# Performance work log

Hardware: AMD Instinct MI355X
Metric: run time of the kernel (lower is better)

The kernel has to match this reference:

```python
import jax, jax.numpy as jnp
import numpy as np

ALG_DIM = 248      # dim of E8 adjoint rep
NNZ_BASE = 300     # base structure-constant triples (antisymmetrized -> 600 nnz)
N_NODES = 20000
N_EDGES = 160000


def _structure_constants():
    """Deterministic sparse antisymmetric structure constants C_ijk.

    Returns index arrays (ci, cj, ck) int32 and values cv float32 such that
    [x, y]_k = sum_t cv[t] * x[ci[t]] * y[cj[t]] with C antisymmetric in (i, j).
    """
    rng = np.random.default_rng(0)
    i = rng.integers(0, ALG_DIM, NNZ_BASE)
    j = rng.integers(0, ALG_DIM, NNZ_BASE)
    j = np.where(j == i, (j + 1) % ALG_DIM, j)  # bracket of equal basis elts is 0
    k = rng.integers(0, ALG_DIM, NNZ_BASE)
    v = rng.normal(size=NNZ_BASE).astype(np.float32)
    ci = np.concatenate([i, j]).astype(np.int32)
    cj = np.concatenate([j, i]).astype(np.int32)
    ck = np.concatenate([k, k]).astype(np.int32)
    cv = np.concatenate([v, -v]).astype(np.float32)
    return jnp.asarray(ci), jnp.asarray(cj), jnp.asarray(ck), jnp.asarray(cv)


def _bracket(x, y, ci, cj, ck, cv):
    """Sparse Lie bracket [x, y]: x, y have shape (..., ALG_DIM)."""
    terms = x[..., ci] * y[..., cj] * cv          # (..., nnz)
    return jnp.zeros(x.shape, x.dtype).at[..., ck].add(terms)


def setup_inputs() -> dict:
    key = jax.random.key(0)
    k1, k2 = jax.random.split(key)
    features = jax.random.normal(k1, (N_NODES, ALG_DIM), dtype=jnp.float32)
    edge_index = jax.random.randint(k2, (2, N_EDGES), 0, N_NODES, dtype=jnp.int32)
    ci, cj, ck, cv = _structure_constants()
    return {
        "features": features,
        "edge_index": edge_index,
        "ci": ci, "cj": cj, "ck": ck, "cv": cv,
        "alpha_msg": jnp.float32(1.0),     # msg_projection.alpha
        "alpha_bil": jnp.float32(1.0),     # msg_bilinear.alpha
        "alpha_w": jnp.float32(1.0),       # update_W.alpha
        "update_scale": jnp.float32(0.1),
    }


def reference(features, edge_index, ci, cj, ck, cv,
              alpha_msg, alpha_bil, alpha_w, update_scale):
    src_idx = edge_index[0]
    tgt_idx = edge_index[1]
    src = features[src_idx]                        # (E, d) gather
    tgt = features[tgt_idx]                        # (E, d) gather
    # message: alpha_bil * [alpha_msg * src, tgt]
    msg = alpha_bil * _bracket(alpha_msg * src, tgt, ci, cj, ck, cv)
    # scatter-add aggregate into per-node accumulator
    agg = jnp.zeros_like(features).at[tgt_idx].add(msg)
    # bracket-based update: x + agg + scale * [agg, alpha_w * agg]
    upd = _bracket(agg, alpha_w * agg, ci, cj, ck, cv)
    return features + agg + update_scale * upd
```

## Files before the change

### kernel.cpp

```cpp
#include <hip/hip_runtime.h>


#define ALG    248
#define ALG4    62
#define PIT2    64
#define SLOTS   32
#define WPB      4
#define NBLK  2048
#define TPL     10
#define NPAD   640

__device__ __forceinline__ unsigned bf16rne(float f) {
    const unsigned u = __float_as_uint(f);
    return (u + 0x7fffu + ((u >> 16) & 1u)) >> 16;
}

__global__ __launch_bounds__(256) void elc_fill(
    const int* __restrict__ ei, int E, int N,
    int* __restrict__ cnt, int* __restrict__ slot,
    const float* __restrict__ feat, uint2* __restrict__ bfeat,
    const int* __restrict__ ci, const int* __restrict__ cj,
    const int* __restrict__ ck, const float* __restrict__ cv,
    int* __restrict__ g_tij, float* __restrict__ g_tv, int nnz)
{
    const int tid = threadIdx.x;

    if (blockIdx.x == 0) {
        __shared__ int   s_cnt[256];
        __shared__ int   s_scan[256];
        __shared__ int   s_cur[256];
        __shared__ int   ls_k[NPAD];
        __shared__ int   ls_ij[NPAD];
        __shared__ float ls_v[NPAD];

        s_cnt[tid] = 0;
        for (int t = tid; t < NPAD; t += 256) { ls_k[t] = 0; ls_ij[t] = 0; ls_v[t] = 0.f; }
        __syncthreads();
        for (int t = tid; t < nnz; t += 256) atomicAdd(&s_cnt[ck[t]], 1);
        __syncthreads();
        int v = s_cnt[tid];
        s_scan[tid] = v;
        __syncthreads();
        for (int off = 1; off < 256; off <<= 1) {
            int u = (tid >= off) ? s_scan[tid - off] : 0;
            __syncthreads();
            s_scan[tid] += u;
            __syncthreads();
        }
        s_cur[tid] = s_scan[tid] - v;
        __syncthreads();
        for (int t = tid; t < nnz; t += 256) {
            const int k = ck[t];
            const int p = atomicAdd(&s_cur[k], 1);
            ls_k[p]  = k;
            ls_ij[p] = ci[t] | (cj[t] << 8);
            ls_v[p]  = cv[t];
        }
        __syncthreads();
        for (int p = tid; p < NPAD; p += 256) {
            const int k  = ls_k[p];
            const int fl = (p + 1 < NPAD && ls_k[p + 1] == k) ? 0 : 1;
            const int w  = ls_ij[p] | (k << 16) | (fl << 24);
            const int phys = (p % TPL) * 64 + (p / TPL);
            g_tij[phys] = w;
            g_tv[phys]  = ls_v[p];
        }
    }

    for (int e = blockIdx.x * 256 + tid; e < E; e += gridDim.x * 256) {
        const int t = ei[E + e];
        const int p = atomicAdd(&cnt[t], 1);
        if (p < SLOTS) slot[t * SLOTS + p] = ei[e];
    }

    const float4* feat4 = (const float4*)feat;
    const int items = N * PIT2;
    for (int it = blockIdx.x * 256 + tid; it < items; it += gridDim.x * 256) {
        const int n = it >> 6;
        const int g = it & 63;
        uint2 o = make_uint2(0u, 0u);
        if (g < ALG4) {
            const float4 f = feat4[(size_t)n * ALG4 + g];
            o.x = bf16rne(f.x) | (bf16rne(f.y) << 16);
            o.y = bf16rne(f.z) | (bf16rne(f.w) << 16);
        }
        bfeat[(size_t)n * PIT2 + g] = o;
    }
}

__global__ __launch_bounds__(256) void elc_node(
    const float* __restrict__ feat,
    const uint2* __restrict__ bfeat,
    const int*   __restrict__ cnt,
    const int*   __restrict__ slot,
    const int*   __restrict__ g_tij,
    const float* __restrict__ g_tv,
    const float* __restrict__ p_am, const float* __restrict__ p_ab,
    const float* __restrict__ p_aw, const float* __restrict__ p_us,
    float* __restrict__ out, int N)
{
    __shared__ __align__(16) float s_tg[WPB][ALG];
    __shared__ __align__(16) float s_S[WPB][ALG];
    __shared__ float s_ag[WPB][ALG];

    const int tid  = threadIdx.x;
    const int lane = tid & 63;
    const int wave = tid >> 6;
    const float4* feat4 = (const float4*)feat;

    int   tw[TPL];
    float tv[TPL];
#pragma unroll
    for (int d = 0; d < TPL; ++d) {
        tw[d] = g_tij[d * 64 + lane];
        tv[d] = g_tv[d * 64 + lane];
    }

    const float cab   = (*p_ab) * (*p_am);
    const float scale = (*p_us) * (*p_aw);

    float* tg = s_tg[wave];
    float* S  = s_S[wave];
    float* ag = s_ag[wave];

    const int stride = NBLK * WPB;
    int n = blockIdx.x * WPB + wave;

    int deg_c = 0, sn_c = 0;
    float4 tgt_c = make_float4(0.f, 0.f, 0.f, 0.f);
    if (n < N) {
        deg_c = min(cnt[n], SLOTS);
        sn_c  = slot[n * SLOTS + (lane & 31)];
        if (lane < ALG4) tgt_c = feat4[(size_t)n * ALG4 + lane];
    }

    int    nP   = -1;
    float4 accP = make_float4(0.f, 0.f, 0.f, 0.f);
    float4 tgtP = make_float4(0.f, 0.f, 0.f, 0.f);

    while (true) {
        const bool have_cur = (n < N);
        const int  n_next   = n + stride;

        uint2 f[8];
        if (have_cur) {
#pragma unroll
            for (int d = 0; d < 8; ++d) {
                f[d] = make_uint2(0u, 0u);
                const int sd = __shfl(sn_c, d);
                if (d < deg_c && lane < ALG4)
                    f[d] = bfeat[(size_t)sd * PIT2 + lane];
            }
        }

        int deg_n = 0, sn_n = 0;
        float4 tgt_n = make_float4(0.f, 0.f, 0.f, 0.f);
        if (have_cur && n_next < N) {
            deg_n = min(cnt[n_next], SLOTS);
            sn_n  = slot[n_next * SLOTS + (lane & 31)];
            if (lane < ALG4) tgt_n = feat4[(size_t)n_next * ALG4 + lane];
        }

        if (nP >= 0) {
            if (lane < ALG4) {
                ((float4*)tg)[lane] = tgtP;
                ((float4*)S)[lane]  = accP;
            }
#pragma unroll
            for (int q = 0; q < 4; ++q) {
                const int k = lane + 64 * q;
                if (k < ALG) ag[k] = 0.f;
            }
            float acc = 0.f;
#pragma unroll
            for (int d = 0; d < TPL; ++d) {
                const int w = tw[d];
                const int i = w & 255;
                const int j = (w >> 8) & 255;
                acc = fmaf(tv[d] * S[i], tg[j], acc);
                if ((w & (1 << 24)) || d == TPL - 1) {
                    atomicAdd(&ag[(w >> 16) & 255], cab * acc);
                    acc = 0.f;
                }
            }
#pragma unroll
            for (int q = 0; q < 4; ++q) {
                const int k = lane + 64 * q;
                if (k < ALG) S[k] = tg[k] + ag[k];
            }
            float acc2 = 0.f;
#pragma unroll
            for (int d = 0; d < TPL; ++d) {
                const int w = tw[d];
                const int i = w & 255;
                const int j = (w >> 8) & 255;
                acc2 = fmaf(tv[d] * ag[i], ag[j], acc2);
                if ((w & (1 << 24)) || d == TPL - 1) {
                    atomicAdd(&S[(w >> 16) & 255], scale * acc2);
                    acc2 = 0.f;
                }
            }
#pragma unroll
            for (int q = 0; q < 4; ++q) {
                const int k = lane + 64 * q;
                if (k < ALG)
                    out[(size_t)nP * ALG + k] = S[k];
            }
        }

        if (!have_cur) break;

        float4 acc = make_float4(0.f, 0.f, 0.f, 0.f);
#pragma unroll
        for (int d = 0; d < 8; ++d) {
            acc.x += __uint_as_float(f[d].x << 16);
            acc.y += __uint_as_float(f[d].x & 0xffff0000u);
            acc.z += __uint_as_float(f[d].y << 16);
            acc.w += __uint_as_float(f[d].y & 0xffff0000u);
        }
        for (int d = 8; d < deg_c; ++d) {
            const int sd = __shfl(sn_c, d);
            if (lane < ALG4) {
                const uint2 fd = bfeat[(size_t)sd * PIT2 + lane];
                acc.x += __uint_as_float(fd.x << 16);
                acc.y += __uint_as_float(fd.x & 0xffff0000u);
                acc.z += __uint_as_float(fd.y << 16);
                acc.w += __uint_as_float(fd.y & 0xffff0000u);
            }
        }

        nP = n; accP = acc; tgtP = tgt_c;
        n = n_next; deg_c = deg_n; sn_c = sn_n; tgt_c = tgt_n;
    }
}

extern "C" void kernel_launch(void* const* d_in, const int* in_sizes, int n_in,
                              void* d_out, int out_size, void* d_ws, size_t ws_size,
                              hipStream_t stream) {
    const float* feat = (const float*)d_in[0];
    const int*   ei   = (const int*)d_in[1];
    const int*   ci   = (const int*)d_in[2];
    const int*   cj   = (const int*)d_in[3];
    const int*   ck   = (const int*)d_in[4];
    const float* cv   = (const float*)d_in[5];
    const float* p_am = (const float*)d_in[6];
    const float* p_ab = (const float*)d_in[7];
    const float* p_aw = (const float*)d_in[8];
    const float* p_us = (const float*)d_in[9];
    float* out = (float*)d_out;

    const int N   = in_sizes[0] / ALG;
    const int E   = in_sizes[1] / 2;
    const int nnz = in_sizes[5];

    char* w = (char*)d_ws;
    int*   g_tij = (int*)w;               w += (size_t)NPAD * sizeof(int);
    float* g_tv  = (float*)w;             w += (size_t)NPAD * sizeof(float);
    int*   cnt   = (int*)w;               w += (size_t)N * sizeof(int);
    int*   slot  = (int*)w;               w += (size_t)N * SLOTS * sizeof(int);
    uint2* bfeat = (uint2*)w;

    hipMemsetAsync(cnt, 0, (size_t)N * sizeof(int), stream);

    elc_fill<<<1024, 256, 0, stream>>>(ei, E, N, cnt, slot, feat, bfeat,
                                       ci, cj, ck, cv, g_tij, g_tv, nnz);
    elc_node<<<NBLK, 256, 0, stream>>>(feat, bfeat, cnt, slot, g_tij, g_tv,
                                       p_am, p_ab, p_aw, p_us, out, N);
}
```

Before: 164.0 us.

## Split fill kernel, read target features as bf16, halve waves per block

Splits the combined setup kernel into separate pack, convert and bucket kernels. The node kernel now reads target-node features from the bf16 copy instead of fp32, halving that traffic, and runs with 2 waves per block over twice as many blocks. This adds kernel launches and loses precision on target features, which may also affect the residual output term.

Result: no change. 166.8 us (+1.7%).

```diff
diff --git a/kernel.cpp b/kernel.cpp
--- a/kernel.cpp
+++ b/kernel.cpp
@@ -5,8 +5,8 @@
 #define ALG4    62
 #define PIT2    64
 #define SLOTS   32
-#define WPB      4
-#define NBLK  2048
+#define WPB      2
+#define NBLK  4096
 #define TPL     10
 #define NPAD   640
 
@@ -15,67 +15,60 @@
     return (u + 0x7fffu + ((u >> 16) & 1u)) >> 16;
 }
 
-__global__ __launch_bounds__(256) void elc_fill(
-    const int* __restrict__ ei, int E, int N,
-    int* __restrict__ cnt, int* __restrict__ slot,
-    const float* __restrict__ feat, uint2* __restrict__ bfeat,
+__global__ __launch_bounds__(256) void elc_pack(
     const int* __restrict__ ci, const int* __restrict__ cj,
     const int* __restrict__ ck, const float* __restrict__ cv,
     int* __restrict__ g_tij, float* __restrict__ g_tv, int nnz)
 {
+    __shared__ int   s_cnt[256];
+    __shared__ int   s_scan[256];
+    __shared__ int   s_cur[256];
+    __shared__ int   ls_k[NPAD];
+    __shared__ int   ls_ij[NPAD];
+    __shared__ float ls_v[NPAD];
     const int tid = threadIdx.x;
 
-    if (blockIdx.x == 0) {
-        __shared__ int   s_cnt[256];
-        __shared__ int   s_scan[256];
-        __shared__ int   s_cur[256];
-        __shared__ int   ls_k[NPAD];
-        __shared__ int   ls_ij[NPAD];
-        __shared__ float ls_v[NPAD];
-
-        s_cnt[tid] = 0;
-        for (int t = tid; t < NPAD; t += 256) { ls_k[t] = 0; ls_ij[t] = 0; ls_v[t] = 0.f; }
+    s_cnt[tid] = 0;
+    for (int t = tid; t < NPAD; t += 256) { ls_k[t] = 0; ls_ij[t] = 0; ls_v[t] = 0.f; }
+    __syncthreads();
+    for (int t = tid; t < nnz; t += 256) atomicAdd(&s_cnt[ck[t]], 1);
+    __syncthreads();
+    int v = s_cnt[tid];
+    s_scan[tid] = v;
+    __syncthreads();
+    for (int off = 1; off < 256; off <<= 1) {
+        int u = (tid >= off) ? s_scan[tid - off] : 0;
         __syncthreads();
-        for (int t = tid; t < nnz; t += 256) atomicAdd(&s_cnt[ck[t]], 1);
+        s_scan[tid] += u;
         __syncthreads();
-        int v = s_cnt[tid];
-        s_scan[tid] = v;
-        __syncthreads();
-        for (int off = 1; off < 256; off <<= 1) {
-            int u = (tid >= off) ? s_scan[tid - off] : 0;
-            __syncthreads();
-            s_scan[tid] += u;
-            __syncthreads();
-        }
-        s_cur[tid] = s_scan[tid] - v;
-        __syncthreads();
-        for (int t = tid; t < nnz; t += 256) {
-            const int k = ck[t];
-            const int p = atomicAdd(&s_cur[k], 1);
-            ls_k[p]  = k;
-            ls_ij[p] = ci[t] | (cj[t] << 8);
-            ls_v[p]  = cv[t];
-        }
-        __syncthreads();
-        for (int p = tid; p < NPAD; p += 256) {
-            const int k  = ls_k[p];
-            const int fl = (p + 1 < NPAD && ls_k[p + 1] == k) ? 0 : 1;
-            const int w  = ls_ij[p] | (k << 16) | (fl << 24);
-            const int phys = (p % TPL) * 64 + (p / TPL);
-            g_tij[phys] = w;
-            g_tv[phys]  = ls_v[p];
-        }
-    }
-
-    for (int e = blockIdx.x * 256 + tid; e < E; e += gridDim.x * 256) {
-        const int t = ei[E + e];
-        const int p = atomicAdd(&cnt[t], 1);
-        if (p < SLOTS) slot[t * SLOTS + p] = ei[e];
-    }
-
+    }
+    s_cur[tid] = s_scan[tid] - v;
+    __syncthreads();
+    for (int t = tid; t < nnz; t += 256) {
+        const int k = ck[t];
+        const int p = atomicAdd(&s_cur[k], 1);
+        ls_k[p]  = k;
+        ls_ij[p] = ci[t] | (cj[t] << 8);
+        ls_v[p]  = cv[t];
+    }
+    __syncthreads();
+    for (int p = tid; p < NPAD; p += 256) {
+        const int k  = ls_k[p];
+        const int fl = (p + 1 < NPAD && ls_k[p + 1] == k) ? 0 : 1;
+        const int w  = ls_ij[p] | (k << 16) | (fl << 24);
+        const int phys = (p % TPL) * 64 + (p / TPL);
+        g_tij[phys] = w;
+        g_tv[phys]  = ls_v[p];
+    }
+}
+
+__global__ __launch_bounds__(256) void elc_convert(
+    const float* __restrict__ feat, uint2* __restrict__ bfeat, int N)
+{
     const float4* feat4 = (const float4*)feat;
     const int items = N * PIT2;
-    for (int it = blockIdx.x * 256 + tid; it < items; it += gridDim.x * 256) {
+    for (int it = blockIdx.x * 256 + threadIdx.x; it < items;
+         it += gridDim.x * 256) {
         const int n = it >> 6;
         const int g = it & 63;
         uint2 o = make_uint2(0u, 0u);
@@ -88,8 +81,18 @@
     }
 }
 
-__global__ __launch_bounds__(256) void elc_node(
-    const float* __restrict__ feat,
+__global__ __launch_bounds__(256) void elc_bucket(
+    const int* __restrict__ ei, int E,
+    int* __restrict__ cnt, int* __restrict__ slot)
+{
+    for (int e = blockIdx.x * 256 + threadIdx.x; e < E; e += gridDim.x * 256) {
+        const int t = ei[E + e];
+        const int p = atomicAdd(&cnt[t], 1);
+        if (p < SLOTS) slot[t * SLOTS + p] = ei[e];
+    }
+}
+
+__global__ __launch_bounds__(128) void elc_node(
     const uint2* __restrict__ bfeat,
     const int*   __restrict__ cnt,
     const int*   __restrict__ slot,
@@ -106,7 +109,6 @@
     const int tid  = threadIdx.x;
     const int lane = tid & 63;
     const int wave = tid >> 6;
-    const float4* feat4 = (const float4*)feat;
 
     int   tw[TPL];
     float tv[TPL];
@@ -127,16 +129,16 @@
     int n = blockIdx.x * WPB + wave;
 
     int deg_c = 0, sn_c = 0;
-    float4 tgt_c = make_float4(0.f, 0.f, 0.f, 0.f);
+    uint2 tgt_c = make_uint2(0u, 0u);
     if (n < N) {
         deg_c = min(cnt[n], SLOTS);
         sn_c  = slot[n * SLOTS + (lane & 31)];
-        if (lane < ALG4) tgt_c = feat4[(size_t)n * ALG4 + lane];
-    }
-
-    int    nP   = -1;
+        if (lane < ALG4) tgt_c = bfeat[(size_t)n * PIT2 + lane];
+    }
+
+    int   nP   = -1;
     float4 accP = make_float4(0.f, 0.f, 0.f, 0.f);
-    float4 tgtP = make_float4(0.f, 0.f, 0.f, 0.f);
+    uint2  tgtP = make_uint2(0u, 0u);
 
     while (true) {
         const bool have_cur = (n < N);
@@ -154,16 +156,21 @@
         }
 
         int deg_n = 0, sn_n = 0;
-        float4 tgt_n = make_float4(0.f, 0.f, 0.f, 0.f);
+        uint2 tgt_n = make_uint2(0u, 0u);
         if (have_cur && n_next < N) {
             deg_n = min(cnt[n_next], SLOTS);
             sn_n  = slot[n_next * SLOTS + (lane & 31)];
-            if (lane < ALG4) tgt_n = feat4[(size_t)n_next * ALG4 + lane];
+            if (lane < ALG4) tgt_n = bfeat[(size_t)n_next * PIT2 + lane];
         }
 
         if (nP >= 0) {
             if (lane < ALG4) {
-                ((float4*)tg)[lane] = tgtP;
+                float4 tf;
+                tf.x = __uint_as_float(tgtP.x << 16);
+                tf.y = __uint_as_float(tgtP.x & 0xffff0000u);
+                tf.z = __uint_as_float(tgtP.y << 16);
+                tf.w = __uint_as_float(tgtP.y & 0xffff0000u);
+                ((float4*)tg)[lane] = tf;
                 ((float4*)S)[lane]  = accP;
             }
 #pragma unroll
@@ -262,8 +269,9 @@
 
     hipMemsetAsync(cnt, 0, (size_t)N * sizeof(int), stream);
 
-    elc_fill<<<1024, 256, 0, stream>>>(ei, E, N, cnt, slot, feat, bfeat,
-                                       ci, cj, ck, cv, g_tij, g_tv, nnz);
-    elc_node<<<NBLK, 256, 0, stream>>>(feat, bfeat, cnt, slot, g_tij, g_tv,
+    elc_pack<<<1, 256, 0, stream>>>(ci, cj, ck, cv, g_tij, g_tv, nnz);
+    elc_convert<<<1280, 256, 0, stream>>>(feat, bfeat, N);
+    elc_bucket<<<640, 256, 0, stream>>>(ei, E, cnt, slot);
+    elc_node<<<NBLK, 128, 0, stream>>>(bfeat, cnt, slot, g_tij, g_tv,
                                        p_am, p_ab, p_aw, p_us, out, N);
 }
```
